# Performance work log

Hardware: AMD Instinct MI355X
Metric: run time of the kernel (lower is better)

The kernel has to match this reference:

```python
import jax, jax.numpy as jnp
import numpy as np

N_NODES = 20000
N_EDGES = 200000
N_GRAPHS = 128
EMB = 256
N_LAYERS = 4
NUM_ELEMENTS = 84
RBF_DIM = 10
RBF_CUTOFF = 8.0


def setup_inputs() -> dict:
    key = jax.random.key(0)
    ks = jax.random.split(key, 20)
    inp = {
        'x': jax.random.randint(ks[0], (N_NODES, 1), 0, NUM_ELEMENTS, dtype=jnp.int64) if jax.config.read('jax_enable_x64') else jax.random.randint(ks[0], (N_NODES, 1), 0, NUM_ELEMENTS).astype(jnp.int32),
        'src': jax.random.randint(ks[1], (N_EDGES,), 0, N_NODES).astype(jnp.int32),
        'dst': jax.random.randint(ks[2], (N_EDGES,), 0, N_NODES).astype(jnp.int32),
        'e': jax.random.uniform(ks[3], (N_EDGES, 1), dtype=jnp.float32) * RBF_CUTOFF,
        'i': jnp.sort(jax.random.randint(ks[4], (N_NODES,), 0, N_GRAPHS)).astype(jnp.int32),
    }
    s_emb = 1.0 / np.sqrt(EMB)
    # element embedding table
    inp['emb_table'] = jax.random.normal(ks[5], (NUM_ELEMENTS, EMB), jnp.float32) * s_emb
    # dense_e applied to RBF expansion
    inp['We'] = jax.random.normal(ks[6], (RBF_DIM, EMB), jnp.float32) * (1.0 / np.sqrt(RBF_DIM))
    inp['be'] = jnp.zeros((EMB,), jnp.float32)
    # CGCNN-style gated message passing layers (stacked over layers)
    def w(k):
        return jax.random.normal(k, (N_LAYERS, EMB, EMB), jnp.float32) * s_emb
    inp['Wg_x'] = w(ks[7]); inp['Wg_n'] = w(ks[8]); inp['Wg_e'] = w(ks[9])
    inp['bg'] = jnp.zeros((N_LAYERS, EMB), jnp.float32)
    inp['Wf_x'] = w(ks[10]); inp['Wf_n'] = w(ks[11]); inp['Wf_e'] = w(ks[12])
    inp['bf'] = jnp.zeros((N_LAYERS, EMB), jnp.float32)
    # dense_n: embedding -> 12
    inp['Wn'] = jax.random.normal(ks[13], (EMB, 12), jnp.float32) * s_emb
    inp['bn'] = jnp.zeros((12,), jnp.float32)
    return inp


def _rbf_expand(d):
    # Gaussian radial basis expansion of scalar distances: [E] -> [E, RBF_DIM]
    centers = jnp.linspace(0.0, RBF_CUTOFF, RBF_DIM, dtype=d.dtype)
    width = centers[1] - centers[0]
    return jnp.exp(-(((d[:, None] - centers) / width) ** 2))


def reference(x, src, dst, e, i, emb_table, We, be, Wg_x, Wg_n, Wg_e, bg,
              Wf_x, Wf_n, Wf_e, bf, Wn, bn):
    xn = emb_table[x[:, 0]]                     # [N, EMB] element embedding
    ef = _rbf_expand(e[:, 0]) @ We + be         # [E, EMB] edge features
    for l in range(N_LAYERS):
        h_i = xn[dst]                           # receiver node features [E, EMB]
        h_j = xn[src]                           # sender node features   [E, EMB]
        # gate/filter computed as split matmuls (equivalent to Dense on concat)
        zg = h_i @ Wg_x[l] + h_j @ Wg_n[l] + ef @ Wg_e[l] + bg[l]
        zf = h_i @ Wf_x[l] + h_j @ Wf_n[l] + ef @ Wf_e[l] + bf[l]
        msg = jax.nn.sigmoid(zg) * jax.nn.softplus(zf)   # [E, EMB]
        agg = jax.ops.segment_sum(msg, dst, num_segments=N_NODES)
        xn = agg + xn                           # residual add (in model call)
    xs = xn @ Wn + bn                           # [N, 12]
    sums = jax.ops.segment_sum(xs, i, num_segments=N_GRAPHS)
    cnts = jax.ops.segment_sum(jnp.ones((xs.shape[0], 1), xs.dtype), i,
                               num_segments=N_GRAPHS)
    out = sums / jnp.maximum(cnts, 1.0)         # global average pool per graph
    return out.reshape(N_GRAPHS, 3, 4)
```

## Files before the change

### kernel.cpp

```cpp
#include <hip/hip_runtime.h>
#include <hip/hip_bf16.h>
#include <math.h>

#define NN   20000
#define NE   200000
#define NG   128
#define EMBD 256
#define NL   4
#define RBFD 10
#define TBINS 1024
#define NWAVE 8192
#define GSPL 8

typedef __attribute__((ext_vector_type(8))) short bf16x8;
typedef __attribute__((ext_vector_type(4))) float f32x4;

__device__ __forceinline__ f32x4 up4(uint2 u) {
  f32x4 r;
  r.x = __uint_as_float(u.x << 16);
  r.y = __uint_as_float(u.x & 0xffff0000u);
  r.z = __uint_as_float(u.y << 16);
  r.w = __uint_as_float(u.y & 0xffff0000u);
  return r;
}


__global__ void k_embed(const int* __restrict__ x, const float* __restrict__ emb,
                        float* __restrict__ xn, __hip_bfloat16* __restrict__ xnb) {
  int idx = blockIdx.x * blockDim.x + threadIdx.x;
  if (idx >= NN * (EMBD / 4)) return;
  int n  = idx >> 6;
  int c4 = (idx & 63) << 2;
  float4 v = *(const float4*)(emb + (size_t)x[n] * EMBD + c4);
  *(float4*)(xn + (size_t)n * EMBD + c4) = v;
  __hip_bfloat16* xb = xnb + (size_t)n * EMBD + c4;
  xb[0] = __float2bfloat16(v.x); xb[1] = __float2bfloat16(v.y);
  xb[2] = __float2bfloat16(v.z); xb[3] = __float2bfloat16(v.w);
}

__global__ void k_wsmall(const float* __restrict__ We, const float* __restrict__ be,
                         const float* __restrict__ Wge, const float* __restrict__ bg,
                         const float* __restrict__ Wfe, const float* __restrict__ bf,
                         float* __restrict__ weff, float* __restrict__ beff) {
  int tid = blockIdx.x * blockDim.x + threadIdx.x;
  const int WPER = RBFD * EMBD;
  if (tid < NL * 2 * WPER) {
    int l  = tid / (2 * WPER);
    int r  = tid % (2 * WPER);
    int gf = r / WPER;
    int r2 = r % WPER;
    int k = r2 / EMBD, c = r2 % EMBD;
    const float* W = (gf == 0 ? Wge : Wfe) + (size_t)l * EMBD * EMBD;
    float s = 0.f;
    for (int j = 0; j < EMBD; ++j) s += We[k * EMBD + j] * W[(size_t)j * EMBD + c];
    weff[tid] = s;
  } else {
    int t2 = tid - NL * 2 * WPER;
    if (t2 >= NL * 2 * EMBD) return;
    int l  = t2 / (2 * EMBD);
    int r  = t2 % (2 * EMBD);
    int gf = r / EMBD, c = r % EMBD;
    const float* W = (gf == 0 ? Wge : Wfe) + (size_t)l * EMBD * EMBD;
    const float* b = (gf == 0 ? bg : bf) + (size_t)l * EMBD;
    float s = b[c];
    for (int j = 0; j < EMBD; ++j) s += be[j] * W[(size_t)j * EMBD + c];
    beff[t2] = s;
  }
}

__global__ void k_table(const float* __restrict__ weff, const float* __restrict__ beff,
                        float* __restrict__ tbl) {
  int idx = blockIdx.x * blockDim.x + threadIdx.x;
  if (idx >= NL * (TBINS + 1) * 512) return;
  int l = idx / ((TBINS + 1) * 512);
  int r = idx % ((TBINS + 1) * 512);
  int bin = r >> 9;
  int t = r & 511;
  int gf = t >> 8, c = t & 255;
  float d = (float)bin * (8.0f / (float)TBINS);
  const float* w = weff + ((size_t)(l * 2 + gf) * RBFD) * EMBD + c;
  float s = beff[(size_t)(l * 2 + gf) * EMBD + c];
  const float width = 8.0f / 9.0f;
  #pragma unroll
  for (int k = 0; k < RBFD; ++k) {
    float u = (d - (float)k * width) / width;
    s += __expf(-u * u) * w[(size_t)k * EMBD];
  }
  tbl[idx] = s;
}

__global__ __launch_bounds__(256) void k_wprep(
    const float* __restrict__ Wgx, const float* __restrict__ Wfx,
    const float* __restrict__ Wgn, const float* __restrict__ Wfn,
    __hip_bfloat16* __restrict__ WT) {
  __shared__ float T[64][65];
  int lq = blockIdx.x; int l = lq >> 2, q = lq & 3;
  const float* W = (q == 0 ? Wgx : q == 1 ? Wfx : q == 2 ? Wgn : Wfn) + (size_t)l * 65536;
  int t = blockIdx.y;
  int k0 = (t & 3) * 64, c0 = (t >> 2) * 64;
  #pragma unroll
  for (int i = 0; i < 16; ++i) {
    int idx = threadIdx.x + i * 256;
    int r = idx >> 6, c = idx & 63;
    T[r][c] = W[(size_t)(k0 + r) * 256 + c0 + c];
  }
  __syncthreads();
  __hip_bfloat16* out = WT + ((size_t)lq * 256) * 256;
  #pragma unroll
  for (int i = 0; i < 16; ++i) {
    int idx = threadIdx.x + i * 256;
    int r = idx >> 6, c = idx & 63;
    out[(size_t)(c0 + r) * 256 + k0 + c] = __float2bfloat16(T[c][r]);
  }
}


__global__ void k_hist(const int* __restrict__ dst, int* __restrict__ cnt) {
  int e = blockIdx.x * blockDim.x + threadIdx.x;
  if (e >= NE) return;
  atomicAdd(&cnt[dst[e]], 1);
}

__global__ __launch_bounds__(1024) void k_scan(const int* __restrict__ cnt,
                                               int* __restrict__ roff,
                                               int* __restrict__ cursor) {
  __shared__ int part[1024];
  const int t = threadIdx.x;
  const int CH = 20;
  int base = t * CH;
  int loc[CH];
  int s = 0;
  #pragma unroll
  for (int i = 0; i < CH; ++i) {
    int idx = base + i;
    int v = (idx < NN) ? cnt[idx] : 0;
    loc[i] = s;
    s += v;
  }
  part[t] = s;
  __syncthreads();
  for (int off = 1; off < 1024; off <<= 1) {
    int v = (t >= off) ? part[t - off] : 0;
    __syncthreads();
    part[t] += v;
    __syncthreads();
  }
  int chunkbase = (t == 0) ? 0 : part[t - 1];
  #pragma unroll
  for (int i = 0; i < CH; ++i) {
    int idx = base + i;
    if (idx < NN) {
      int v = chunkbase + loc[i];
      roff[idx] = v;
      cursor[idx] = v;
    }
  }
  if (t == 1023) roff[NN] = part[1023];
}

__global__ void k_scatter(const int* __restrict__ src, const int* __restrict__ dst,
                          const float* __restrict__ edist,
                          int* __restrict__ cursor,
                          int* __restrict__ src_s, float* __restrict__ db_s) {
  int e = blockIdx.x * blockDim.x + threadIdx.x;
  if (e >= NE) return;
  int d = dst[e];
  int p = atomicAdd(&cursor[d], 1);
  src_s[p] = src[e];
  float dd = edist[e] * ((float)TBINS / 8.0f);
  db_s[p] = fminf(fmaxf(dd, 0.0f), (float)TBINS - 0.001f);
}


__global__ __launch_bounds__(256) void k_nodemm(
    const __hip_bfloat16* __restrict__ xnb, const __hip_bfloat16* __restrict__ WTl,
    __hip_bfloat16* __restrict__ Yb) {
  __shared__ unsigned short As[128 * 32];
  __shared__ unsigned short Bs[128 * 32];
  const int tid = threadIdx.x;
  const int lane = tid & 63;
  const int wave = tid >> 6;
  const int row0 = blockIdx.x << 7;
  const int by = blockIdx.y;
  const int col0 = by << 7;
  const int q = col0 >> 8;
  const int cb = col0 & 255;
  const unsigned short* xb = (const unsigned short*)xnb;
  const unsigned short* Wb = (const unsigned short*)WTl + ((size_t)q * 256 + cb) * 256;
  const int wr = (wave >> 1) << 6;
  const int wc = (wave & 1) << 6;
  f32x4 acc[4][4] = {};

  for (int k0 = 0; k0 < 256; k0 += 32) {
    #pragma unroll
    for (int h = 0; h < 2; ++h) {
      int c = tid + (h << 8);
      int r = c >> 2, s = c & 3;
      int sw = s ^ ((r >> 1) & 3);
      int ga = row0 + r; if (ga > NN - 1) ga = NN - 1;
      *(bf16x8*)(&As[r * 32 + sw * 8]) =
          *(const bf16x8*)(xb + (size_t)ga * 256 + k0 + s * 8);
      *(bf16x8*)(&Bs[r * 32 + sw * 8]) =
          *(const bf16x8*)(Wb + (size_t)r * 256 + k0 + s * 8);
    }
    __syncthreads();
    bf16x8 af[4], bfr[4];
    const int rsel = lane & 15, ksl = lane >> 4;
    #pragma unroll
    for (int m = 0; m < 4; ++m) {
      int r = wr + m * 16 + rsel;
      int sw = ksl ^ ((r >> 1) & 3);
      af[m] = *(const bf16x8*)(&As[r * 32 + sw * 8]);
    }
    #pragma unroll
    for (int n = 0; n < 4; ++n) {
      int r = wc + n * 16 + rsel;
      int sw = ksl ^ ((r >> 1) & 3);
      bfr[n] = *(const bf16x8*)(&Bs[r * 32 + sw * 8]);
    }
    #pragma unroll
    for (int m = 0; m < 4; ++m)
      #pragma unroll
      for (int n = 0; n < 4; ++n)
        acc[m][n] = __builtin_amdgcn_mfma_f32_16x16x32_bf16(af[m], bfr[n], acc[m][n], 0, 0, 0);
    __syncthreads();
  }

  const int crow = (lane >> 4) << 2;
  const int ccol = lane & 15;
  #pragma unroll
  for (int m = 0; m < 4; ++m)
    #pragma unroll
    for (int j = 0; j < 4; ++j) {
      int gr = row0 + wr + m * 16 + crow + j;
      if (gr < NN) {
        #pragma unroll
        for (int n = 0; n < 4; ++n)
          Yb[(size_t)gr * 1024 + col0 + wc + n * 16 + ccol] = __float2bfloat16(acc[m][n][j]);
      }
    }
}

__device__ __forceinline__ float gate1(float zg, float zf) {
  float sg = __builtin_amdgcn_rcpf(1.0f + __expf(-zg));
  float sp = fmaxf(zf, 0.0f) + __logf(1.0f + __expf(-fabsf(zf)));
  return sg * sp;
}

__global__ __launch_bounds__(256, 8) void k_agg(
    const __hip_bfloat16* __restrict__ Yb, const int* __restrict__ roff,
    const int* __restrict__ src_s, const float* __restrict__ db_s,
    const float* __restrict__ tblL,
    float* __restrict__ xn, __hip_bfloat16* __restrict__ xnb) {
  const int wave = threadIdx.x >> 6, lane = threadIdx.x & 63;
  const int c4 = lane << 2;
  const int wid0 = blockIdx.x * 4 + wave;

  for (int n = wid0; n < NN; n += NWAVE) {
    const int jb   = __builtin_amdgcn_readfirstlane(roff[n]);
    const int jend = __builtin_amdgcn_readfirstlane(roff[n + 1]);
    const int deg = jend - jb;

    const unsigned short* yrow = (const unsigned short*)Yb + (size_t)n * 1024 + c4;
    f32x4 bgv = up4(*(const uint2*)(yrow));
    f32x4 bfv = up4(*(const uint2*)(yrow + 256));

    f32x4 m4 = {};
    if (deg > 0) {
      const int dcap = deg < 64 ? deg : 64;
      int sv = 0; int bv = 0; int fv = 0;
      if (lane < dcap) {
        sv = src_s[jb + lane];
        float db = db_s[jb + lane];
        int b = (int)db;
        bv = b;
        fv = __float_as_int(db - (float)b);
      }
      const unsigned short* Ysrc = (const unsigned short*)Yb + c4 + 512;
      for (int i = 0; i < dcap; ++i) {
        int sn = __builtin_amdgcn_readlane(sv, i);
        int bn = __builtin_amdgcn_readlane(bv, i);
        float fr = __int_as_float(__builtin_amdgcn_readlane(fv, i));
        const unsigned short* ys = Ysrc + (size_t)sn * 1024;
        uint2 pa = *(const uint2*)(ys);
        uint2 pf = *(const uint2*)(ys + 256);
        const float* tp = tblL + (size_t)bn * 512 + c4;
        f32x4 t0g = *(const f32x4*)(tp);
        f32x4 t0f = *(const f32x4*)(tp + 256);
        f32x4 t1g = *(const f32x4*)(tp + 512);
        f32x4 t1f = *(const f32x4*)(tp + 768);
        f32x4 zg = bgv + up4(pa) + t0g + fr * (t1g - t0g);
        f32x4 zf = bfv + up4(pf) + t0f + fr * (t1f - t0f);
        m4.x += gate1(zg.x, zf.x);
        m4.y += gate1(zg.y, zf.y);
        m4.z += gate1(zg.z, zf.z);
        m4.w += gate1(zg.w, zf.w);
      }
      for (int i = 64; i < deg; ++i) {
        int sn = src_s[jb + i];
        float db = db_s[jb + i];
        int bn = (int)db;
        float fr = db - (float)bn;
        const unsigned short* ys = Ysrc + (size_t)sn * 1024;
        uint2 pa = *(const uint2*)(ys);
        uint2 pf = *(const uint2*)(ys + 256);
        const float* tp = tblL + (size_t)bn * 512 + c4;
        f32x4 t0g = *(const f32x4*)(tp);
        f32x4 t0f = *(const f32x4*)(tp + 256);
        f32x4 t1g = *(const f32x4*)(tp + 512);
        f32x4 t1f = *(const f32x4*)(tp + 768);
        f32x4 zg = bgv + up4(pa) + t0g + fr * (t1g - t0g);
        f32x4 zf = bfv + up4(pf) + t0f + fr * (t1f - t0f);
        m4.x += gate1(zg.x, zf.x);
        m4.y += gate1(zg.y, zf.y);
        m4.z += gate1(zg.z, zf.z);
        m4.w += gate1(zg.w, zf.w);
      }
    }
    float4 xv = *(const float4*)(xn + (size_t)n * EMBD + c4);
    xv.x += m4.x; xv.y += m4.y; xv.z += m4.z; xv.w += m4.w;
    *(float4*)(xn + (size_t)n * EMBD + c4) = xv;
    __hip_bfloat16* xbp = xnb + (size_t)n * EMBD + c4;
    xbp[0] = __float2bfloat16(xv.x); xbp[1] = __float2bfloat16(xv.y);
    xbp[2] = __float2bfloat16(xv.z); xbp[3] = __float2bfloat16(xv.w);
  }
}


__global__ __launch_bounds__(256) void k_gsum(
    const float* __restrict__ xn, const int* __restrict__ gi,
    float* __restrict__ gpart, float* __restrict__ gcnt) {
  const int g = blockIdx.x, p = blockIdx.y;
  int lo = 0, hi = NN;
  while (lo < hi) { int m = (lo + hi) >> 1; if (gi[m] < g) lo = m + 1; else hi = m; }
  int lo2 = lo, hi2 = NN;
  while (lo2 < hi2) { int m = (lo2 + hi2) >> 1; if (gi[m] < g + 1) lo2 = m + 1; else hi2 = m; }
  const int cntv = lo2 - lo;
  const int r0 = lo + (cntv * p) / GSPL;
  const int r1 = lo + (cntv * (p + 1)) / GSPL;
  const int c = threadIdx.x;
  float acc = 0.f;
  for (int r = r0; r < r1; ++r) acc += xn[(size_t)r * EMBD + c];
  gpart[((size_t)g * GSPL + p) * EMBD + c] = acc;
  if (p == 0 && c == 0) gcnt[g] = (float)cntv;
}

__global__ __launch_bounds__(256) void k_final(
    const float* __restrict__ gpart, const float* __restrict__ gcnt,
    const float* __restrict__ Wn, const float* __restrict__ bn,
    float* __restrict__ out) {
  __shared__ float s[EMBD];
  const int g = blockIdx.x;
  const int c = threadIdx.x;
  float v = 0.f;
  #pragma unroll
  for (int p = 0; p < GSPL; ++p) v += gpart[((size_t)g * GSPL + p) * EMBD + c];
  s[c] = v;
  __syncthreads();
  if (c < 12) {
    float acc = 0.f;
    for (int k = 0; k < EMBD; ++k) acc += s[k] * Wn[k * 12 + c];
    float cv = gcnt[g];
    out[g * 12 + c] = (cv > 0.f) ? acc / cv + bn[c] : 0.f;
  }
}


extern "C" void kernel_launch(void* const* d_in, const int* in_sizes, int n_in,
                              void* d_out, int out_size, void* d_ws, size_t ws_size,
                              hipStream_t stream) {
  const int*   x   = (const int*)d_in[0];
  const int*   src = (const int*)d_in[1];
  const int*   dst = (const int*)d_in[2];
  const float* e   = (const float*)d_in[3];
  const int*   gi  = (const int*)d_in[4];
  const float* emb = (const float*)d_in[5];
  const float* We  = (const float*)d_in[6];
  const float* be  = (const float*)d_in[7];
  const float* Wgx = (const float*)d_in[8];
  const float* Wgn = (const float*)d_in[9];
  const float* Wge = (const float*)d_in[10];
  const float* bg  = (const float*)d_in[11];
  const float* Wfx = (const float*)d_in[12];
  const float* Wfn = (const float*)d_in[13];
  const float* Wfe = (const float*)d_in[14];
  const float* bf  = (const float*)d_in[15];
  const float* Wn  = (const float*)d_in[16];
  const float* bn  = (const float*)d_in[17];
  float* out = (float*)d_out;

  char* ws = (char*)d_ws;
  size_t off = 0;
  auto alloc = [&](size_t bytes) {
    void* p = ws + off;
    off += (bytes + 255) & ~(size_t)255;
    return p;
  };
  float*           xn    = (float*)alloc((size_t)NN * EMBD * 4);
  __hip_bfloat16*  xnb   = (__hip_bfloat16*)alloc((size_t)NN * EMBD * 2);
  __hip_bfloat16*  Yb    = (__hip_bfloat16*)alloc((size_t)NN * 1024 * 2);
  float*           db_s  = (float*)alloc((size_t)NE * 4);
  int*             src_s = (int*)alloc((size_t)NE * 4);
  int*             cnt   = (int*)alloc((size_t)NN * 4);
  int*             roff  = (int*)alloc((size_t)(NN + 1) * 4);
  int*             curs  = (int*)alloc((size_t)NN * 4);
  float*           weff  = (float*)alloc((size_t)NL * 2 * RBFD * EMBD * 4);
  float*           beff  = (float*)alloc((size_t)NL * 2 * EMBD * 4);
  float*           tbl   = (float*)alloc((size_t)NL * (TBINS + 1) * 512 * 4);
  __hip_bfloat16*  WT    = (__hip_bfloat16*)alloc((size_t)NL * 4 * 256 * 256 * 2);
  float*           gpart = (float*)alloc((size_t)NG * GSPL * EMBD * 4);
  float*           gcnt  = (float*)alloc((size_t)NG * 4);
  (void)ws_size; (void)in_sizes; (void)n_in; (void)out_size;

  hipMemsetAsync(cnt, 0, (size_t)NN * 4, stream);

  k_embed<<<(NN * (EMBD / 4) + 255) / 256, 256, 0, stream>>>(x, emb, xn, xnb);
  k_wsmall<<<(NL * 2 * (RBFD + 1) * EMBD + 255) / 256, 256, 0, stream>>>(
      We, be, Wge, bg, Wfe, bf, weff, beff);
  k_table<<<(NL * (TBINS + 1) * 512 + 255) / 256, 256, 0, stream>>>(weff, beff, tbl);
  k_wprep<<<dim3(NL * 4, 16), 256, 0, stream>>>(Wgx, Wfx, Wgn, Wfn, WT);
  k_hist<<<(NE + 255) / 256, 256, 0, stream>>>(dst, cnt);
  k_scan<<<1, 1024, 0, stream>>>(cnt, roff, curs);
  k_scatter<<<(NE + 255) / 256, 256, 0, stream>>>(src, dst, e, curs, src_s, db_s);

  dim3 mmgrid((NN + 127) / 128, 8);
  for (int l = 0; l < NL; ++l) {
    k_nodemm<<<mmgrid, 256, 0, stream>>>(xnb, WT + (size_t)l * 4 * 65536, Yb);
    k_agg<<<NWAVE / 4, 256, 0, stream>>>(
        Yb, roff, src_s, db_s, tbl + (size_t)l * (TBINS + 1) * 512, xn, xnb);
  }
  k_gsum<<<dim3(NG, GSPL), 256, 0, stream>>>(xn, gi, gpart, gcnt);
  k_final<<<NG, 256, 0, stream>>>(gpart, gcnt, Wn, bn, out);
}
```

Baseline: 490.4 us.

## Use direct global-to-LDS loads, BK=64, and transposed MFMA for packed stores

Rewrites the node GEMM tile loader to use global_load_lds 16-byte transfers straight into shared memory, doubling the K step to 64 with a new XOR swizzle. The MFMA operands are swapped so each lane holds four consecutive output channels, which lets the epilogue write packed 4×bf16 stores instead of scalar 2-byte stores. The aim is to cut VGPR staging, loop iterations and scattered store traffic, at the cost of twice the LDS per block and reliance on the LDS-DMA path layout being correct.

```diff
diff --git a/kernel.cpp b/kernel.cpp
--- a/kernel.cpp
+++ b/kernel.cpp
@@ -22,6 +22,17 @@
   r.z = __uint_as_float(u.y << 16);
   r.w = __uint_as_float(u.y & 0xffff0000u);
   return r;
+}
+
+__device__ __forceinline__ void gload16(const void* g, void* l) {
+  __builtin_amdgcn_global_load_lds(
+      (const __attribute__((address_space(1))) void*)g,
+      (__attribute__((address_space(3))) void*)l, 16, 0, 0);
+}
+
+__device__ __forceinline__ unsigned short bfbits(float v) {
+  __hip_bfloat16 h = __float2bfloat16(v);
+  return *(unsigned short*)&h;
 }
 
 
@@ -175,70 +186,78 @@
 __global__ __launch_bounds__(256) void k_nodemm(
     const __hip_bfloat16* __restrict__ xnb, const __hip_bfloat16* __restrict__ WTl,
     __hip_bfloat16* __restrict__ Yb) {
-  __shared__ unsigned short As[128 * 32];
-  __shared__ unsigned short Bs[128 * 32];
+  __shared__ unsigned short As[128 * 64];
+  __shared__ unsigned short Bs[128 * 64];
   const int tid = threadIdx.x;
   const int lane = tid & 63;
   const int wave = tid >> 6;
   const int row0 = blockIdx.x << 7;
-  const int by = blockIdx.y;
-  const int col0 = by << 7;
+  const int col0 = blockIdx.y << 7;
   const int q = col0 >> 8;
   const int cb = col0 & 255;
   const unsigned short* xb = (const unsigned short*)xnb;
   const unsigned short* Wb = (const unsigned short*)WTl + ((size_t)q * 256 + cb) * 256;
-  const int wr = (wave >> 1) << 6;
-  const int wc = (wave & 1) << 6;
+  const int wnode = (wave >> 1) << 6;
+  const int wch   = (wave & 1) << 6;
   f32x4 acc[4][4] = {};
 
-  for (int k0 = 0; k0 < 256; k0 += 32) {
+  const int rd0 = (wave << 3) + (lane >> 3);
+  const int cd  = lane & 7;
+
+  for (int k0 = 0; k0 < 256; k0 += 64) {
+    #pragma unroll
+    for (int j = 0; j < 4; ++j) {
+      int rd = rd0 + j * 32;
+      int cs = cd ^ (rd & 7);
+      int ga = row0 + rd; if (ga > NN - 1) ga = NN - 1;
+      gload16(xb + (size_t)ga * 256 + k0 + cs * 8,
+              (char*)As + (size_t)(j * 256 + wave * 64) * 16);
+      gload16(Wb + (size_t)rd * 256 + k0 + cs * 8,
+              (char*)Bs + (size_t)(j * 256 + wave * 64) * 16);
+    }
+    __syncthreads();
+    const int rsel = lane & 15, ksl = lane >> 4;
     #pragma unroll
     for (int h = 0; h < 2; ++h) {
-      int c = tid + (h << 8);
-      int r = c >> 2, s = c & 3;
-      int sw = s ^ ((r >> 1) & 3);
-      int ga = row0 + r; if (ga > NN - 1) ga = NN - 1;
-      *(bf16x8*)(&As[r * 32 + sw * 8]) =
-          *(const bf16x8*)(xb + (size_t)ga * 256 + k0 + s * 8);
-      *(bf16x8*)(&Bs[r * 32 + sw * 8]) =
-          *(const bf16x8*)(Wb + (size_t)r * 256 + k0 + s * 8);
+      const int c = h * 4 + ksl;
+      bf16x8 xa[4], wf[4];
+      #pragma unroll
+      for (int nn = 0; nn < 4; ++nn) {
+        int r = wnode + nn * 16 + rsel;
+        xa[nn] = *(const bf16x8*)(&As[r * 64 + (c ^ (r & 7)) * 8]);
+      }
+      #pragma unroll
+      for (int mc = 0; mc < 4; ++mc) {
+        int r = wch + mc * 16 + rsel;
+        wf[mc] = *(const bf16x8*)(&Bs[r * 64 + (c ^ (r & 7)) * 8]);
+      }
+      #pragma unroll
+      for (int mc = 0; mc < 4; ++mc)
+        #pragma unroll
+        for (int nn = 0; nn < 4; ++nn)
+          acc[mc][nn] = __builtin_amdgcn_mfma_f32_16x16x32_bf16(wf[mc], xa[nn], acc[mc][nn], 0, 0, 0);
     }
     __syncthreads();
-    bf16x8 af[4], bfr[4];
-    const int rsel = lane & 15, ksl = lane >> 4;
+  }
+
+  const int nodesel = lane & 15;
+  const int chq = (lane >> 4) << 2;
+  #pragma unroll
+  for (int mc = 0; mc < 4; ++mc) {
     #pragma unroll
-    for (int m = 0; m < 4; ++m) {
-      int r = wr + m * 16 + rsel;
-      int sw = ksl ^ ((r >> 1) & 3);
-      af[m] = *(const bf16x8*)(&As[r * 32 + sw * 8]);
+    for (int nn = 0; nn < 4; ++nn) {
+      int node = row0 + wnode + nn * 16 + nodesel;
+      if (node < NN) {
+        int ch = col0 + wch + mc * 16 + chq;
+        ushort4 pk;
+        pk.x = bfbits(acc[mc][nn][0]);
+        pk.y = bfbits(acc[mc][nn][1]);
+        pk.z = bfbits(acc[mc][nn][2]);
+        pk.w = bfbits(acc[mc][nn][3]);
+        *(ushort4*)((unsigned short*)Yb + (size_t)node * 1024 + ch) = pk;
+      }
     }
-    #pragma unroll
-    for (int n = 0; n < 4; ++n) {
-      int r = wc + n * 16 + rsel;
-      int sw = ksl ^ ((r >> 1) & 3);
-      bfr[n] = *(const bf16x8*)(&Bs[r * 32 + sw * 8]);
-    }
-    #pragma unroll
-    for (int m = 0; m < 4; ++m)
-      #pragma unroll
-      for (int n = 0; n < 4; ++n)
-        acc[m][n] = __builtin_amdgcn_mfma_f32_16x16x32_bf16(af[m], bfr[n], acc[m][n], 0, 0, 0);
-    __syncthreads();
-  }
-
-  const int crow = (lane >> 4) << 2;
-  const int ccol = lane & 15;
-  #pragma unroll
-  for (int m = 0; m < 4; ++m)
-    #pragma unroll
-    for (int j = 0; j < 4; ++j) {
-      int gr = row0 + wr + m * 16 + crow + j;
-      if (gr < NN) {
-        #pragma unroll
-        for (int n = 0; n < 4; ++n)
-          Yb[(size_t)gr * 1024 + col0 + wc + n * 16 + ccol] = __float2bfloat16(acc[m][n][j]);
-      }
-    }
+  }
 }
 
 __device__ __forceinline__ float gate1(float zg, float zf) {
```

Result: no change. 488.5 us (-0.4%).
